# Performance work log

Hardware: AMD Instinct MI355X
Metric: run time of the kernel (lower is better)

The kernel has to match this reference:

```python
import jax, jax.numpy as jnp
import numpy as np

B, S, H, NH = 2, 2048, 768, 12
HD = H // NH
SCALE = HD ** -0.5


def setup_inputs() -> dict:
    key = jax.random.key(0)
    ks = jax.random.split(key, 12)
    std = H ** -0.5
    return {
        "hidden_states": jax.random.normal(ks[0], (B, S, H), jnp.float32),
        "aspect_weights": jax.random.normal(ks[1], (B, S), jnp.float32),
        "opinion_weights": jax.random.normal(ks[2], (B, S), jnp.float32),
        "attention_mask": jnp.ones((B, S), jnp.int32),
        # stacked params, branch axis order: 0=aspect, 1=opinion, 2=context
        "Wq": jax.random.normal(ks[3], (3, H, H), jnp.float32) * std,
        "bq": jax.random.normal(ks[4], (3, H), jnp.float32) * 0.02,
        "Wk": jax.random.normal(ks[5], (3, H, H), jnp.float32) * std,
        "bk": jax.random.normal(ks[6], (3, H), jnp.float32) * 0.02,
        "Wv": jax.random.normal(ks[7], (3, H, H), jnp.float32) * std,
        "bv": jax.random.normal(ks[8], (3, H), jnp.float32) * 0.02,
        "Wo": jax.random.normal(ks[9], (3, H, H), jnp.float32) * std,
        "bo": jax.random.normal(ks[10], (3, H), jnp.float32) * 0.02,
    }


def _proj(x, W, b):
    # x: [B,S,H], W: [3,H,H], b: [3,H] -> [3,B,nh,S,hd]
    y = jnp.einsum("bsh,nhe->nbse", x, W) + b[:, None, None, :]
    return y.reshape(3, x.shape[0], x.shape[1], NH, HD).transpose(0, 1, 3, 2, 4)


def reference(hidden_states, aspect_weights, opinion_weights, attention_mask,
              Wq, bq, Wk, bk, Wv, bv, Wo, bo):
    q = _proj(hidden_states, Wq, bq)  # [3,B,nh,S,hd]
    k = _proj(hidden_states, Wk, bk)
    v = _proj(hidden_states, Wv, bv)

    mask = (attention_mask == 0)[:, None, None, :]  # [B,1,1,S], True = masked

    def masked_softmax(scores):
        scores = jnp.where(mask, -jnp.inf, scores)
        return jax.nn.softmax(scores, axis=-1)

    scores = jnp.einsum("nbhqd,nbhkd->nbhqk", q, k) * SCALE  # [3,B,nh,S,S]

    a_bias = aspect_weights[:, None, :, None]   # [B,1,S,1] per-query bias
    o_bias = opinion_weights[:, None, :, None]

    p_a = masked_softmax(scores[0] + a_bias)                     # [B,nh,S,S]
    p_o = masked_softmax(scores[1] + o_bias)
    p_c = masked_softmax(scores[2] + 0.5 * (p_a + p_o))

    probs = jnp.stack([p_a, p_o, p_c])                           # [3,B,nh,S,S]
    ctx = jnp.einsum("nbhqk,nbhkd->nbhqd", probs, v)             # [3,B,nh,S,hd]
    ctx = ctx.transpose(0, 1, 3, 2, 4).reshape(3, hidden_states.shape[0], hidden_states.shape[1], H)
    out = jnp.einsum("nbsh,nhe->nbse", ctx, Wo) + bo[:, None, None, :]
    return (out[0], out[1], out[2])
```

## Files before the change

### kernel.cpp

```cpp
#include <hip/hip_runtime.h>
#include <hip/hip_bf16.h>

#define DI __device__ __forceinline__

typedef __bf16 bf16;
typedef bf16  bf16x8 __attribute__((ext_vector_type(8)));
typedef bf16  bf16x4 __attribute__((ext_vector_type(4)));
typedef float f32x4  __attribute__((ext_vector_type(4)));
typedef unsigned int u32x4 __attribute__((ext_vector_type(4)));

static constexpr int Bb = 2, Ss = 2048, Hh = 768, NHh = 12, HDd = 64;
static constexpr float SL2 = 0.125f * 1.4426950408889634f;
static constexpr float C2  = 0.5f   * 1.4426950408889634f;

DI f32x4 zero4() { f32x4 z = {0.f, 0.f, 0.f, 0.f}; return z; }

__global__ __launch_bounds__(256) void conv_x(const float* __restrict__ x,
                                              bf16* __restrict__ xb) {
  int i = blockIdx.x * 256 + threadIdx.x;
  float4 v = ((const float4*)x)[i];
  bf16x4 o;
  o[0] = (bf16)v.x; o[1] = (bf16)v.y; o[2] = (bf16)v.z; o[3] = (bf16)v.w;
  ((bf16x4*)xb)[i] = o;
}

__global__ __launch_bounds__(256) void transpose_w(
    const float* __restrict__ Wq, const float* __restrict__ Wk,
    const float* __restrict__ Wv, const float* __restrict__ Wo,
    bf16* __restrict__ dst) {
  __shared__ float t[32][33];
  const int z = blockIdx.z;
  const int set = z / 3, n = z - set * 3;
  const float* src = (set == 0) ? Wq : (set == 1) ? Wk : (set == 2) ? Wv : Wo;
  src += (size_t)n * Hh * Hh;
  bf16* out = dst + ((size_t)set * 3 + n) * Hh * Hh;
  const int e0 = blockIdx.x * 32, h0 = blockIdx.y * 32;
  const int tx = threadIdx.x, ty = threadIdx.y;
#pragma unroll
  for (int i = 0; i < 4; i++)
    t[ty + 8 * i][tx] = src[(size_t)(h0 + ty + 8 * i) * Hh + e0 + tx];
  __syncthreads();
#pragma unroll
  for (int i = 0; i < 4; i++)
    out[(size_t)(e0 + ty + 8 * i) * Hh + h0 + tx] = (bf16)t[tx][ty + 8 * i];
}

DI void gemm_core128(const bf16* __restrict__ A, const bf16* __restrict__ Bm,
                     int m0, int n0, bf16 (*As)[40], bf16 (*Bs)[40],
                     f32x4 acc[4][4]) {
  const int tid = threadIdx.x;
  const int lane = tid & 63, lg = lane >> 4, lc = lane & 15;
  const int wr = tid >> 7, wc = (tid >> 6) & 1;
  for (int k0 = 0; k0 < Hh; k0 += 32) {
    __syncthreads();
#pragma unroll
    for (int i = 0; i < 2; i++) {
      int c = tid + i * 256;
      int r = c >> 2, o = (c & 3) * 8;
      *(u32x4*)&As[r][o] = *(const u32x4*)&A[(size_t)(m0 + r) * Hh + k0 + o];
      *(u32x4*)&Bs[r][o] = *(const u32x4*)&Bm[(size_t)(n0 + r) * Hh + k0 + o];
    }
    __syncthreads();
    bf16x8 a[4], b[4];
#pragma unroll
    for (int i = 0; i < 4; i++)
      a[i] = *(const bf16x8*)&As[wr * 64 + i * 16 + lc][lg * 8];
#pragma unroll
    for (int i = 0; i < 4; i++)
      b[i] = *(const bf16x8*)&Bs[wc * 64 + i * 16 + lc][lg * 8];
#pragma unroll
    for (int mi = 0; mi < 4; mi++)
#pragma unroll
      for (int ni = 0; ni < 4; ni++)
        acc[mi][ni] = __builtin_amdgcn_mfma_f32_16x16x32_bf16(
            a[mi], b[ni], acc[mi][ni], 0, 0, 0);
  }
}

__global__ __launch_bounds__(256) void gemm_qkv(
    const bf16* __restrict__ xb, const bf16* __restrict__ Wt,
    const float* __restrict__ bq, const float* __restrict__ bk,
    const float* __restrict__ bv, bf16* __restrict__ qo,
    bf16* __restrict__ ko, bf16* __restrict__ vo) {
  __shared__ bf16 As[128][40], Bs[128][40];
  const int mt = blockIdx.x, nt = blockIdx.y, z = blockIdx.z;
  const int proj = z / 3, n = z - proj * 3;
  const bf16* Wm = Wt + ((size_t)proj * 3 + n) * Hh * Hh;
  const float* bias = ((proj == 0) ? bq : (proj == 1) ? bk : bv) + n * Hh;
  f32x4 acc[4][4];
#pragma unroll
  for (int mi = 0; mi < 4; mi++)
#pragma unroll
    for (int ni = 0; ni < 4; ni++) acc[mi][ni] = zero4();
  gemm_core128(xb, Wm, mt * 128, nt * 128, As, Bs, acc);

  const int tid = threadIdx.x, lane = tid & 63, lg = lane >> 4, lc = lane & 15;
  const int wr = tid >> 7, wc = (tid >> 6) & 1;
  const int rbase = mt * 128 + wr * 64 + lg * 4;
  const int cbase = nt * 128 + wc * 64 + lc;
  if (proj < 2) {
    bf16* out = (proj == 0) ? qo : ko;
#pragma unroll
    for (int ni = 0; ni < 4; ni++) {
      int e = cbase + ni * 16, hi = e >> 6, d = e & 63;
      float bval = bias[e];
#pragma unroll
      for (int mi = 0; mi < 4; mi++) {
        int row = rbase + mi * 16;
        int bidx = row >> 11, ss = row & 2047;
        size_t p = (((size_t)(n * Bb + bidx) * NHh + hi) * Ss + ss) * HDd + d;
#pragma unroll
        for (int r = 0; r < 4; r++)
          out[p + (size_t)r * HDd] = (bf16)(acc[mi][ni][r] + bval);
      }
    }
  } else {
#pragma unroll
    for (int ni = 0; ni < 4; ni++) {
      int e = cbase + ni * 16, hi = e >> 6, d = e & 63;
      float bval = bias[e];
#pragma unroll
      for (int mi = 0; mi < 4; mi++) {
        int row = rbase + mi * 16;
        int bidx = row >> 11, ss = row & 2047;
        bf16x4 pk;
#pragma unroll
        for (int r = 0; r < 4; r++) pk[r] = (bf16)(acc[mi][ni][r] + bval);
        *(bf16x4*)&vo[(((size_t)(n * Bb + bidx) * NHh + hi) * HDd + d) * Ss + ss] = pk;
      }
    }
  }
}

__global__ __launch_bounds__(256) void gemm_out_k(
    const bf16* __restrict__ ctx, const bf16* __restrict__ Wto,
    const float* __restrict__ bo, float* __restrict__ out) {
  __shared__ bf16 As[128][40], Bs[128][40];
  const int mt = blockIdx.x, nt = blockIdx.y;
  const int n = mt >> 5;
  const bf16* Wm = Wto + (size_t)n * Hh * Hh;
  const float* bias = bo + n * Hh;
  f32x4 acc[4][4];
#pragma unroll
  for (int mi = 0; mi < 4; mi++)
#pragma unroll
    for (int ni = 0; ni < 4; ni++) acc[mi][ni] = zero4();
  gemm_core128(ctx, Wm, mt * 128, nt * 128, As, Bs, acc);

  const int tid = threadIdx.x, lane = tid & 63, lg = lane >> 4, lc = lane & 15;
  const int wr = tid >> 7, wc = (tid >> 6) & 1;
  const int rbase = mt * 128 + wr * 64 + lg * 4;
  const int cbase = nt * 128 + wc * 64 + lc;
#pragma unroll
  for (int ni = 0; ni < 4; ni++) {
    int col = cbase + ni * 16;
    float bval = bias[col];
#pragma unroll
    for (int mi = 0; mi < 4; mi++) {
      int row = rbase + mi * 16;
#pragma unroll
      for (int r = 0; r < 4; r++)
        out[(size_t)(row + r) * Hh + col] = acc[mi][ni][r] + bval;
    }
  }
}

__global__ __launch_bounds__(256, 3) void attn_kernel(
    const bf16* __restrict__ q, const bf16* __restrict__ k,
    const bf16* __restrict__ vT, bf16* __restrict__ ctx) {
  __shared__ __align__(16) bf16 smem[24576];

  const int tid = threadIdx.x;
  const int lane = tid & 63, w = tid >> 6;
  const int lg = lane >> 4, lc = lane & 15;
  const int qt = blockIdx.x, bh = blockIdx.y;
  const int bidx = bh / NHh, hidx = bh - bidx * NHh;
  const int swk = (lc & 7) << 3;

  size_t base[3];
#pragma unroll
  for (int n = 0; n < 3; n++)
    base[n] = ((size_t)(n * Bb + bidx) * NHh + hidx) * (size_t)(Ss * HDd);

  const int qr = qt * 64 + w * 16;

  bf16x8 qf[3][2];
#pragma unroll
  for (int n = 0; n < 3; n++)
#pragma unroll
    for (int sl = 0; sl < 2; sl++)
      qf[n][sl] = *(const bf16x8*)&q[base[n] + (size_t)(qr + lc) * HDd + sl * 32 + lg * 8];

  auto stage_k = [&](int kt0, int nmax) {
#pragma unroll
    for (int i = 0; i < 6; i++) {
      int n_ = i >> 1;
      if (n_ >= nmax) break;
      int rem = (i & 1) * 256 + tid;
      int rr = rem >> 3, o8 = (rem & 7) << 3;
      *(u32x4*)&smem[n_ * 4096 + rr * 64 + (o8 ^ ((rr & 7) << 3))] =
          *(const u32x4*)&k[base[n_] + (size_t)(kt0 + rr) * HDd + o8];
    }
  };
  auto stage_v = [&](int kt0) {
#pragma unroll
    for (int i = 0; i < 6; i++) {
      int n_ = i >> 1;
      int rem = (i & 1) * 256 + tid;
      int rr = rem >> 3, o8 = (rem & 7) << 3;
      *(u32x4*)&smem[12288 + n_ * 4096 + rr * 64 + (o8 ^ ((rr & 7) << 3))] =
          *(const u32x4*)&vT[base[n_] + (size_t)rr * Ss + kt0 + o8];
    }
  };

  auto qkt = [&](int n_, f32x4 s[4]) {
    __builtin_amdgcn_s_setprio(1);
#pragma unroll
    for (int t = 0; t < 4; t++) {
      int row = t * 16 + lc;
      bf16x8 a0 = *(const bf16x8*)&smem[n_ * 4096 + row * 64 + ((lg * 8) ^ swk)];
      bf16x8 a1 = *(const bf16x8*)&smem[n_ * 4096 + row * 64 + ((32 + lg * 8) ^ swk)];
      s[t] = __builtin_amdgcn_mfma_f32_16x16x32_bf16(a0, qf[n_][0], s[t], 0, 0, 0);
      s[t] = __builtin_amdgcn_mfma_f32_16x16x32_bf16(a1, qf[n_][1], s[t], 0, 0, 0);
    }
    __builtin_amdgcn_s_setprio(0);
  };

  auto tilestat = [&](const f32x4 s[4], float& m, float& l) {
    float tm = -3.4e38f;
#pragma unroll
    for (int t = 0; t < 4; t++)
#pragma unroll
      for (int r = 0; r < 4; r++) tm = fmaxf(tm, s[t][r]);
    tm *= SL2;
    tm = fmaxf(tm, __shfl_xor(tm, 16));
    tm = fmaxf(tm, __shfl_xor(tm, 32));
    float nm = fmaxf(m, tm);
    float sum = 0.f;
#pragma unroll
    for (int t = 0; t < 4; t++)
#pragma unroll
      for (int r = 0; r < 4; r++)
        sum += __builtin_amdgcn_exp2f(fmaf(s[t][r], SL2, -nm));
    sum += __shfl_xor(sum, 16);
    sum += __shfl_xor(sum, 32);
    l = l * __builtin_amdgcn_exp2f(m - nm) + sum;
    m = nm;
  };

  auto pv = [&](int n_, const f32x4 p[4], f32x4 cacc[4]) {
    const bf16* vb = &smem[12288 + n_ * 4096];
    bf16x8 vf0[4], vf1[4];
#pragma unroll
    for (int t = 0; t < 4; t++) {
      int row = t * 16 + lc;
      vf0[t] = *(const bf16x8*)&vb[row * 64 + ((lg * 8) ^ swk)];
      vf1[t] = *(const bf16x8*)&vb[row * 64 + ((32 + lg * 8) ^ swk)];
    }
#pragma unroll
    for (int t = 0; t < 4; t++) {
      bf16x4 pk;
#pragma unroll
      for (int r = 0; r < 4; r++) pk[r] = (bf16)p[t][r];
      int slot = 2 * t + (lg >> 1);
      int swz = ((slot ^ (lc & 7)) << 3) + 4 * (lg & 1);
      *(bf16x4*)&smem[(w * 16 + lc) * 64 + swz] = pk;
    }
    asm volatile("s_waitcnt lgkmcnt(0)" ::: "memory");
    __builtin_amdgcn_sched_barrier(0);
    bf16x8 pfa = *(const bf16x8*)&smem[(w * 16 + lc) * 64 + ((lg ^ (lc & 7)) << 3)];
    bf16x8 pfb = *(const bf16x8*)&smem[(w * 16 + lc) * 64 + (((4 + lg) ^ (lc & 7)) << 3)];
    __builtin_amdgcn_s_setprio(1);
#pragma unroll
    for (int t = 0; t < 4; t++) {
      cacc[t] = __builtin_amdgcn_mfma_f32_16x16x32_bf16(pfa, vf0[t], cacc[t], 0, 0, 0);
      cacc[t] = __builtin_amdgcn_mfma_f32_16x16x32_bf16(pfb, vf1[t], cacc[t], 0, 0, 0);
    }
    __builtin_amdgcn_s_setprio(0);
  };

  float m0 = -3.4e38f, l0 = 0.f, m1 = -3.4e38f, l1 = 0.f;
  for (int kt = 0; kt < Ss; kt += 64) {
    __syncthreads();
    stage_k(kt, 2);
    __syncthreads();
    {
      f32x4 s[4] = {zero4(), zero4(), zero4(), zero4()};
      qkt(0, s);
      tilestat(s, m0, l0);
    }
    {
      f32x4 s[4] = {zero4(), zero4(), zero4(), zero4()};
      qkt(1, s);
      tilestat(s, m1, l1);
    }
  }
  const float mm0 = m0 + __builtin_amdgcn_logf(l0);
  const float mm1 = m1 + __builtin_amdgcn_logf(l1);

  f32x4 c0[4], c1[4], c2[4];
#pragma unroll
  for (int t = 0; t < 4; t++) { c0[t] = zero4(); c1[t] = zero4(); c2[t] = zero4(); }
  float m2 = -1e30f, l2 = 0.f;

  for (int kt = 0; kt < Ss; kt += 64) {
    __syncthreads();
    stage_k(kt, 3);
    stage_v(kt);
    __syncthreads();
    f32x4 pa[4], po[4], p2[4];
    {
      f32x4 s[4] = {zero4(), zero4(), zero4(), zero4()};
      qkt(0, s);
#pragma unroll
      for (int t = 0; t < 4; t++)
#pragma unroll
        for (int r = 0; r < 4; r++)
          pa[t][r] = __builtin_amdgcn_exp2f(fmaf(s[t][r], SL2, -mm0));
    }
    {
      f32x4 s[4] = {zero4(), zero4(), zero4(), zero4()};
      qkt(1, s);
#pragma unroll
      for (int t = 0; t < 4; t++)
#pragma unroll
        for (int r = 0; r < 4; r++)
          po[t][r] = __builtin_amdgcn_exp2f(fmaf(s[t][r], SL2, -mm1));
    }
    {
      f32x4 s[4] = {zero4(), zero4(), zero4(), zero4()};
      qkt(2, s);
#pragma unroll
      for (int t = 0; t < 4; t++)
#pragma unroll
        for (int r = 0; r < 4; r++)
          p2[t][r] = fmaf(s[t][r], SL2, (pa[t][r] + po[t][r]) * C2);
      float tm = -3.4e38f;
#pragma unroll
      for (int t = 0; t < 4; t++)
#pragma unroll
        for (int r = 0; r < 4; r++) tm = fmaxf(tm, p2[t][r]);
      tm = fmaxf(tm, __shfl_xor(tm, 16));
      tm = fmaxf(tm, __shfl_xor(tm, 32));
      if (!__all(tm <= m2 + 8.f)) {
        float nm = fmaxf(m2, tm);
        float al = __builtin_amdgcn_exp2f(m2 - nm);
        float ab[4];
#pragma unroll
        for (int r = 0; r < 4; r++) ab[r] = __shfl(al, 4 * lg + r, 64);
#pragma unroll
        for (int t = 0; t < 4; t++)
#pragma unroll
          for (int r = 0; r < 4; r++) c2[t][r] *= ab[r];
        l2 *= al;
        m2 = nm;
      }
      float sum = 0.f;
#pragma unroll
      for (int t = 0; t < 4; t++)
#pragma unroll
        for (int r = 0; r < 4; r++) {
          p2[t][r] = __builtin_amdgcn_exp2f(p2[t][r] - m2);
          sum += p2[t][r];
        }
      sum += __shfl_xor(sum, 16);
      sum += __shfl_xor(sum, 32);
      l2 += sum;
    }
    __syncthreads();
    pv(0, pa, c0);
    pv(1, po, c1);
    pv(2, p2, c2);
  }

  {
    float il2 = 1.f / l2;
    float ib[4];
#pragma unroll
    for (int r = 0; r < 4; r++) ib[r] = __shfl(il2, 4 * lg + r, 64);
#pragma unroll
    for (int t = 0; t < 4; t++)
#pragma unroll
      for (int r = 0; r < 4; r++) c2[t][r] *= ib[r];
  }
#pragma unroll
  for (int n = 0; n < 3; n++) {
    const f32x4* cc = (n == 0) ? c0 : (n == 1) ? c1 : c2;
#pragma unroll
    for (int t = 0; t < 4; t++)
#pragma unroll
      for (int r = 0; r < 4; r++)
        ctx[((size_t)(n * Bb + bidx) * Ss + qr + 4 * lg + r) * Hh + hidx * HDd +
            t * 16 + lc] = (bf16)cc[t][r];
  }
}

extern "C" void kernel_launch(void* const* d_in, const int* in_sizes, int n_in,
                              void* d_out, int out_size, void* d_ws,
                              size_t ws_size, hipStream_t stream) {
  const float* x  = (const float*)d_in[0];
  const float* Wq = (const float*)d_in[4];
  const float* bq = (const float*)d_in[5];
  const float* Wk = (const float*)d_in[6];
  const float* bk = (const float*)d_in[7];
  const float* Wv = (const float*)d_in[8];
  const float* bv = (const float*)d_in[9];
  const float* Wo = (const float*)d_in[10];
  const float* bo = (const float*)d_in[11];
  float* out = (float*)d_out;

  char* ws = (char*)d_ws;
  bf16* xb  = (bf16*)(ws);
  bf16* Wt  = (bf16*)(ws + 6291456);
  bf16* qb  = (bf16*)(ws + 20447232);
  bf16* kb  = (bf16*)(ws + 39321600);
  bf16* vtb = (bf16*)(ws + 58195968);
  bf16* ctx = (bf16*)(ws + 77070336);

  conv_x<<<3072, 256, 0, stream>>>(x, xb);
  transpose_w<<<dim3(24, 24, 12), dim3(32, 8), 0, stream>>>(Wq, Wk, Wv, Wo, Wt);
  gemm_qkv<<<dim3(32, 6, 9), 256, 0, stream>>>(xb, Wt, bq, bk, bv, qb, kb, vtb);
  attn_kernel<<<dim3(32, 24), 256, 0, stream>>>(qb, kb, vtb, ctx);
  gemm_out_k<<<dim3(96, 6), 256, 0, stream>>>(ctx, Wt + (size_t)3 * 3 * 768 * 768,
                                              bo, out);
}
```

Before: 429.7 us.

## Prefetch next tiles into registers in GEMM and attention loops, remap attention grid

The GEMM core and both attention passes now issue the next tile's global loads into registers before computing on the current shared-memory tile, then commit them to LDS after compute. The goal is to overlap global-load latency with MFMA work instead of stalling at the top of each iteration. The attention grid is flattened to 1D with a remapping that interleaves heads across blocks, and launch bounds change (GEMMs to 3 waves/SIMD hint, attention to 2). The trade is higher register pressure from the prefetch buffers, which may cost occupancy, plus an extra barrier pair per iteration.

Measured after the change: 414.9 us. -3.4%, faster.

```diff
diff --git a/kernel.cpp b/kernel.cpp
--- a/kernel.cpp
+++ b/kernel.cpp
@@ -51,16 +51,29 @@
   const int tid = threadIdx.x;
   const int lane = tid & 63, lg = lane >> 4, lc = lane & 15;
   const int wr = tid >> 7, wc = (tid >> 6) & 1;
+  u32x4 ar[2], br[2];
+  auto issue = [&](int k0) {
+#pragma unroll
+    for (int i = 0; i < 2; i++) {
+      int c = tid + i * 256, r = c >> 2, o = (c & 3) * 8;
+      ar[i] = *(const u32x4*)&A[(size_t)(m0 + r) * Hh + k0 + o];
+      br[i] = *(const u32x4*)&Bm[(size_t)(n0 + r) * Hh + k0 + o];
+    }
+  };
+  auto commit = [&]() {
+#pragma unroll
+    for (int i = 0; i < 2; i++) {
+      int c = tid + i * 256, r = c >> 2, o = (c & 3) * 8;
+      *(u32x4*)&As[r][o] = ar[i];
+      *(u32x4*)&Bs[r][o] = br[i];
+    }
+  };
+  issue(0);
+  commit();
+  __syncthreads();
   for (int k0 = 0; k0 < Hh; k0 += 32) {
-    __syncthreads();
-#pragma unroll
-    for (int i = 0; i < 2; i++) {
-      int c = tid + i * 256;
-      int r = c >> 2, o = (c & 3) * 8;
-      *(u32x4*)&As[r][o] = *(const u32x4*)&A[(size_t)(m0 + r) * Hh + k0 + o];
-      *(u32x4*)&Bs[r][o] = *(const u32x4*)&Bm[(size_t)(n0 + r) * Hh + k0 + o];
-    }
-    __syncthreads();
+    const bool more = (k0 + 32 < Hh);
+    if (more) issue(k0 + 32);
     bf16x8 a[4], b[4];
 #pragma unroll
     for (int i = 0; i < 4; i++)
@@ -68,16 +81,23 @@
 #pragma unroll
     for (int i = 0; i < 4; i++)
       b[i] = *(const bf16x8*)&Bs[wc * 64 + i * 16 + lc][lg * 8];
+    __builtin_amdgcn_s_setprio(1);
 #pragma unroll
     for (int mi = 0; mi < 4; mi++)
 #pragma unroll
       for (int ni = 0; ni < 4; ni++)
         acc[mi][ni] = __builtin_amdgcn_mfma_f32_16x16x32_bf16(
             a[mi], b[ni], acc[mi][ni], 0, 0, 0);
-  }
-}
-
-__global__ __launch_bounds__(256) void gemm_qkv(
+    __builtin_amdgcn_s_setprio(0);
+    if (more) {
+      __syncthreads();
+      commit();
+      __syncthreads();
+    }
+  }
+}
+
+__global__ __launch_bounds__(256, 3) void gemm_qkv(
     const bf16* __restrict__ xb, const bf16* __restrict__ Wt,
     const float* __restrict__ bq, const float* __restrict__ bk,
     const float* __restrict__ bv, bf16* __restrict__ qo,
@@ -132,7 +152,7 @@
   }
 }
 
-__global__ __launch_bounds__(256) void gemm_out_k(
+__global__ __launch_bounds__(256, 3) void gemm_out_k(
     const bf16* __restrict__ ctx, const bf16* __restrict__ Wto,
     const float* __restrict__ bo, float* __restrict__ out) {
   __shared__ bf16 As[128][40], Bs[128][40];
@@ -165,7 +185,7 @@
   }
 }
 
-__global__ __launch_bounds__(256, 3) void attn_kernel(
+__global__ __launch_bounds__(256, 2) void attn_kernel(
     const bf16* __restrict__ q, const bf16* __restrict__ k,
     const bf16* __restrict__ vT, bf16* __restrict__ ctx) {
   __shared__ __align__(16) bf16 smem[24576];
@@ -173,7 +193,10 @@
   const int tid = threadIdx.x;
   const int lane = tid & 63, w = tid >> 6;
   const int lg = lane >> 4, lc = lane & 15;
-  const int qt = blockIdx.x, bh = blockIdx.y;
+  const int f = blockIdx.x;
+  const int j = f >> 3;
+  const int bh = (f & 7) * 3 + (j >> 5);
+  const int qt = j & 31;
   const int bidx = bh / NHh, hidx = bh - bidx * NHh;
   const int swk = (lc & 7) << 3;
 
@@ -191,25 +214,44 @@
     for (int sl = 0; sl < 2; sl++)
       qf[n][sl] = *(const bf16x8*)&q[base[n] + (size_t)(qr + lc) * HDd + sl * 32 + lg * 8];
 
-  auto stage_k = [&](int kt0, int nmax) {
-#pragma unroll
-    for (int i = 0; i < 6; i++) {
+  u32x4 kreg[6], vreg[6];
+  auto issueK2 = [&](int kt0) {
+#pragma unroll
+    for (int i = 0; i < 4; i++) {
       int n_ = i >> 1;
-      if (n_ >= nmax) break;
       int rem = (i & 1) * 256 + tid;
       int rr = rem >> 3, o8 = (rem & 7) << 3;
-      *(u32x4*)&smem[n_ * 4096 + rr * 64 + (o8 ^ ((rr & 7) << 3))] =
-          *(const u32x4*)&k[base[n_] + (size_t)(kt0 + rr) * HDd + o8];
-    }
-  };
-  auto stage_v = [&](int kt0) {
+      kreg[i] = *(const u32x4*)&k[base[n_] + (size_t)(kt0 + rr) * HDd + o8];
+    }
+  };
+  auto commitK2 = [&]() {
+#pragma unroll
+    for (int i = 0; i < 4; i++) {
+      int n_ = i >> 1;
+      int rem = (i & 1) * 256 + tid;
+      int rr = rem >> 3, o8 = (rem & 7) << 3;
+      *(u32x4*)&smem[n_ * 4096 + rr * 64 + (o8 ^ ((rr & 7) << 3))] = kreg[i];
+    }
+  };
+  auto issueP2 = [&](int kt0) {
 #pragma unroll
     for (int i = 0; i < 6; i++) {
       int n_ = i >> 1;
       int rem = (i & 1) * 256 + tid;
       int rr = rem >> 3, o8 = (rem & 7) << 3;
-      *(u32x4*)&smem[12288 + n_ * 4096 + rr * 64 + (o8 ^ ((rr & 7) << 3))] =
-          *(const u32x4*)&vT[base[n_] + (size_t)rr * Ss + kt0 + o8];
+      kreg[i] = *(const u32x4*)&k[base[n_] + (size_t)(kt0 + rr) * HDd + o8];
+      vreg[i] = *(const u32x4*)&vT[base[n_] + (size_t)rr * Ss + kt0 + o8];
+    }
+  };
+  auto commitP2 = [&]() {
+#pragma unroll
+    for (int i = 0; i < 6; i++) {
+      int n_ = i >> 1;
+      int rem = (i & 1) * 256 + tid;
+      int rr = rem >> 3, o8 = (rem & 7) << 3;
+      int sw = o8 ^ ((rr & 7) << 3);
+      *(u32x4*)&smem[n_ * 4096 + rr * 64 + sw] = kreg[i];
+      *(u32x4*)&smem[12288 + n_ * 4096 + rr * 64 + sw] = vreg[i];
     }
   };
 
@@ -248,7 +290,7 @@
     m = nm;
   };
 
-  auto pv = [&](int n_, const f32x4 p[4], f32x4 cacc[4]) {
+  auto pv = [&](int n_, const bf16x4 pk[4], f32x4 cacc[4]) {
     const bf16* vb = &smem[12288 + n_ * 4096];
     bf16x8 vf0[4], vf1[4];
 #pragma unroll
@@ -259,12 +301,9 @@
     }
 #pragma unroll
     for (int t = 0; t < 4; t++) {
-      bf16x4 pk;
-#pragma unroll
-      for (int r = 0; r < 4; r++) pk[r] = (bf16)p[t][r];
       int slot = 2 * t + (lg >> 1);
       int swz = ((slot ^ (lc & 7)) << 3) + 4 * (lg & 1);
-      *(bf16x4*)&smem[(w * 16 + lc) * 64 + swz] = pk;
+      *(bf16x4*)&smem[(w * 16 + lc) * 64 + swz] = pk[t];
     }
     asm volatile("s_waitcnt lgkmcnt(0)" ::: "memory");
     __builtin_amdgcn_sched_barrier(0);
@@ -280,10 +319,12 @@
   };
 
   float m0 = -3.4e38f, l0 = 0.f, m1 = -3.4e38f, l1 = 0.f;
+  issueK2(0);
+  commitK2();
+  __syncthreads();
   for (int kt = 0; kt < Ss; kt += 64) {
-    __syncthreads();
-    stage_k(kt, 2);
-    __syncthreads();
+    const bool more = (kt + 64 < Ss);
+    if (more) issueK2(kt + 64);
     {
       f32x4 s[4] = {zero4(), zero4(), zero4(), zero4()};
       qkt(0, s);
@@ -294,7 +335,13 @@
       qkt(1, s);
       tilestat(s, m1, l1);
     }
-  }
+    if (more) {
+      __syncthreads();
+      commitK2();
+      __syncthreads();
+    }
+  }
+  issueP2(0);
   const float mm0 = m0 + __builtin_amdgcn_logf(l0);
   const float mm1 = m1 + __builtin_amdgcn_logf(l1);
 
@@ -303,11 +350,13 @@
   for (int t = 0; t < 4; t++) { c0[t] = zero4(); c1[t] = zero4(); c2[t] = zero4(); }
   float m2 = -1e30f, l2 = 0.f;
 
+  __syncthreads();
+  commitP2();
+  __syncthreads();
   for (int kt = 0; kt < Ss; kt += 64) {
-    __syncthreads();
-    stage_k(kt, 3);
-    stage_v(kt);
-    __syncthreads();
+    const bool more = (kt + 64 < Ss);
+    if (more) issueP2(kt + 64);
+
     f32x4 pa[4], po[4], p2[4];
     {
       f32x4 s[4] = {zero4(), zero4(), zero4(), zero4()};
@@ -367,10 +416,24 @@
       sum += __shfl_xor(sum, 32);
       l2 += sum;
     }
+    bf16x4 pkA[4], pkB[4], pkC[4];
+#pragma unroll
+    for (int t = 0; t < 4; t++)
+#pragma unroll
+      for (int r = 0; r < 4; r++) {
+        pkA[t][r] = (bf16)pa[t][r];
+        pkB[t][r] = (bf16)po[t][r];
+        pkC[t][r] = (bf16)p2[t][r];
+      }
     __syncthreads();
-    pv(0, pa, c0);
-    pv(1, po, c1);
-    pv(2, p2, c2);
+    pv(0, pkA, c0);
+    pv(1, pkB, c1);
+    pv(2, pkC, c2);
+    if (more) {
+      __syncthreads();
+      commitP2();
+      __syncthreads();
+    }
   }
 
   {
@@ -420,7 +483,7 @@
   conv_x<<<3072, 256, 0, stream>>>(x, xb);
   transpose_w<<<dim3(24, 24, 12), dim3(32, 8), 0, stream>>>(Wq, Wk, Wv, Wo, Wt);
   gemm_qkv<<<dim3(32, 6, 9), 256, 0, stream>>>(xb, Wt, bq, bk, bv, qb, kb, vtb);
-  attn_kernel<<<dim3(32, 24), 256, 0, stream>>>(qb, kb, vtb, ctx);
+  attn_kernel<<<768, 256, 0, stream>>>(qb, kb, vtb, ctx);
   gemm_out_k<<<dim3(96, 6), 256, 0, stream>>>(ctx, Wt + (size_t)3 * 3 * 768 * 768,
                                               bo, out);
 }
```
